# Performance work log

Measured on AMD Instinct MI355X. Metric: run time of the kernel, lower is better.

The kernel has to match this reference:

```python
import jax, jax.numpy as jnp
import numpy as np

B, N, L, H = 4, 512, 512, 8
D = 64          # d_model
TAU = 4         # conv dilation
E = 25          # conv kernel size (odd, floor(100/tau))
K = 32          # low_rank_d == top-k
L_OUT = L - TAU * (E - 1)   # 416, n_manifold_embed
EPS = 1e-6


def setup_inputs() -> dict:
    key = jax.random.key(0)
    ks = jax.random.split(key, 7)
    return {
        "x": jax.random.normal(ks[0], (B, N, L, H), jnp.float32),
        "target": jax.random.normal(ks[1], (B, N, L), jnp.float32),
        "conv_w": jax.random.normal(ks[2], (D, H, E), jnp.float32) * 0.05,  # Conv1d weight (out,in,k)
        "proj_w": jax.random.normal(ks[3], (L_OUT,), jnp.float32) * 0.05,   # Linear(L_OUT,1) weight
        "proj_b": jnp.zeros((), jnp.float32),                                # Linear bias
        "W0": jax.random.normal(ks[4], (L, K), jnp.float32) * 0.05,          # low-rank corr proj
        "U0": jax.random.normal(ks[5], (L, K), jnp.float32) * 0.05,
    }


def reference(x, target, conv_w, proj_w, proj_b, W0, U0):
    # --- dilated conv1d manifold embedding: (b n l h) -> ((b n) h l) ---
    xin = jnp.transpose(x.reshape(B * N, L, H), (0, 2, 1))  # (BN, H, L)
    conv = jax.lax.conv_general_dilated(
        xin, conv_w, window_strides=(1,), padding="VALID",
        rhs_dilation=(TAU,), dimension_numbers=("NCH", "OIH", "NCH"))  # (BN, D, L_OUT)
    # conv_out_proj: Linear(L_OUT -> 1) + GELU (exact erf, torch default)
    embed = jax.nn.gelu(conv @ proj_w + proj_b, approximate=False).reshape(B, N, D)

    # --- pearson correlation (computed under no_grad in torch) ---
    v = target - target.mean(axis=-1, keepdims=True)          # (B, N, L)
    vx = v @ W0                                               # (B, N, K)
    vh = v @ U0                                               # (B, N, K)
    num = jnp.einsum("bnk,bmk->bnm", vx, vh)                  # (B, N, N)
    nx = jnp.sqrt(jnp.sum(vx * vx, axis=-1) + EPS)            # (B, N)
    nh = jnp.sqrt(jnp.sum(vh * vh, axis=-1) + EPS)
    pearson = jax.lax.stop_gradient(num / (nx[:, :, None] * nh[:, None, :]))

    # --- top-k sparsification + scatter + softmax normalization ---
    vals, idx = jax.lax.top_k(pearson, K)                     # (B, N, K)
    bi = jnp.arange(B)[:, None, None]
    ni = jnp.arange(N)[None, :, None]
    sparse = jnp.zeros_like(pearson).at[bi, ni, idx].set(vals)  # scatter topk values
    mult = jax.nn.softmax(sparse, axis=-1)                    # F.softmax over full row (zeros included)

    # --- gated attention: sparse correlation graph mixes manifold embeddings ---
    out = jnp.einsum("bnm,bmd->bnd", mult, embed)             # (B, N, D)
    attn = pearson.mean(axis=0)                               # (N, N), returned pearson_cor
    return out, attn
```

## Files before the change

kernel.cpp:

```cpp
#include <hip/hip_runtime.h>
#include <math.h>

#define BB 4
#define NN 512
#define LL 512
#define HH 8
#define DD 64
#define EE 25
#define KK 32
#define LOUT 416
#define EPSF 1e-6f


__global__ void k_transpose_cw(const float* __restrict__ cw, float* __restrict__ Ct) {
    int i = blockIdx.x * 256 + threadIdx.x;
    if (i < DD * HH * EE) {
        int d = i / (HH * EE);
        int he = i % (HH * EE);
        Ct[he * DD + d] = cw[i];
    }
}

__global__ __launch_bounds__(256, 4) void k_fused(
    const float* __restrict__ x, const float* __restrict__ pw,
    const float* __restrict__ pb, const float* __restrict__ Ct,
    float* __restrict__ embedBuf,
    const float* __restrict__ target, const float* __restrict__ W0,
    const float* __restrict__ U0, float* __restrict__ vxn,
    float* __restrict__ vhnT) {
    __shared__ float P[608];
    __shared__ float Sred[4][200];
    __shared__ float Stot[200];
    __shared__ float opart[4][64];
    __shared__ float T[2][512];
    __shared__ float mus[2];
    __shared__ float S2[4][2][64];

    int tid = threadIdx.x;
    int w = tid >> 6, lane = tid & 63;
    int bid = blockIdx.x;
    int sel = bid % 3;

    if (sel != 2) {
        int bn = (bid / 3) * 2 + sel;
        for (int i = tid; i < 608; i += 256) {
            int t = i - 96;
            P[i] = (t >= 0 && t < LOUT) ? pw[t] : 0.f;
        }
        __syncthreads();

        const float* xp = x + (size_t)bn * (LL * HH);
        int q = lane >> 3;
        int jb = 16 * w;

        float W[25];
#pragma unroll
        for (int k = 0; k < 25; ++k) W[k] = P[q + 8 * jb + 4 * k];
        float S[25];
#pragma unroll
        for (int e = 0; e < 25; ++e) S[e] = 0.f;

#pragma unroll
        for (int jl = 0; jl < 16; ++jl) {
            int j = jb + jl;
            float v = xp[64 * j + lane];
#pragma unroll
            for (int k = 0; k < 25; ++k)
                S[24 - k] = fmaf(v, W[k], S[24 - k]);
            if (jl < 15) {
#pragma unroll
                for (int k = 0; k < 23; ++k) W[k] = W[k + 2];
                int l = q + 8 * j;
                W[23] = P[l + 100];
                W[24] = P[l + 104];
            }
        }
#pragma unroll
        for (int e = 0; e < 25; ++e) {
            S[e] += __shfl_xor(S[e], 8);
            S[e] += __shfl_xor(S[e], 16);
            S[e] += __shfl_xor(S[e], 32);
        }
        if (lane < 8) {
#pragma unroll
            for (int e = 0; e < 25; ++e) Sred[w][lane * 25 + e] = S[e];
        }
        __syncthreads();
        if (tid < 200)
            Stot[tid] = Sred[0][tid] + Sred[1][tid] + Sred[2][tid] + Sred[3][tid];
        __syncthreads();

        float acc = 0.f;
#pragma unroll 10
        for (int ii = 0; ii < 50; ++ii) {
            int i = 50 * w + ii;
            acc = fmaf(Ct[i * 64 + lane], Stot[i], acc);
        }
        opart[w][lane] = acc;
        __syncthreads();
        if (w == 0) {
            float a = opart[0][lane] + opart[1][lane] + opart[2][lane]
                    + opart[3][lane] + pb[0];
            float g = 0.5f * a * (1.f + erff(a * 0.70710678118654752f));
            embedBuf[(size_t)bn * 64 + lane] = g;
        }
    } else {
        int r0 = (bid / 3) * 2;
        const float4* tp = (const float4*)(target + (size_t)r0 * 512);
        ((float4*)&T[0][0])[tid] = tp[tid];
        __syncthreads();

        if (w < 2) {
            float s = 0.f;
#pragma unroll
            for (int c = 0; c < 8; ++c) s += T[w][lane + 64 * c];
#pragma unroll
            for (int off = 1; off < 64; off <<= 1) s += __shfl_xor(s, off);
            if (lane == 0) mus[w] = s * (1.f / 512.f);
        }
        __syncthreads();
#pragma unroll
        for (int c = 0; c < 4; ++c) {
            int i = tid + c * 256;
            T[i >> 9][i & 511] -= mus[i >> 9];
        }
        __syncthreads();

        const float* base = (lane < 32) ? W0 : U0;
        int k = lane & 31;
        float acc0 = 0.f, acc1 = 0.f;
        int l0 = w * 128;
#pragma unroll 4
        for (int li = 0; li < 128; ++li) {
            int l = l0 + li;
            float wv = base[l * 32 + k];
            acc0 = fmaf(wv, T[0][l], acc0);
            acc1 = fmaf(wv, T[1][l], acc1);
        }
        S2[w][0][lane] = acc0;
        S2[w][1][lane] = acc1;
        __syncthreads();

        if (w < 2) {
            int r = w;
            float tot = S2[0][r][lane] + S2[1][r][lane] + S2[2][r][lane]
                      + S2[3][r][lane];
            float sq = tot * tot;
#pragma unroll
            for (int off = 1; off < 32; off <<= 1) sq += __shfl_xor(sq, off);
            float o = tot / sqrtf(sq + EPSF);
            int row = r0 + r, b = row >> 9, n = row & 511;
            if (lane < 32) vxn[(size_t)row * 32 + lane] = o;
            else           vhnT[(size_t)b * (32 * 512) + (lane - 32) * 512 + n] = o;
        }
    }
}

__global__ __launch_bounds__(1024) void k_sumembed(
    const float* __restrict__ embedBuf, float* __restrict__ sumEmbed) {
    int b = blockIdx.x, tid = threadIdx.x;
    int d = tid & 63, c = tid >> 6;
    float s = 0.f;
    for (int r = c; r < 512; r += 16)
        s += embedBuf[((size_t)b * 512 + r) * 64 + d];
    __shared__ float red[16][64];
    red[c][d] = s;
    __syncthreads();
    if (c == 0) {
        float t = 0.f;
#pragma unroll
        for (int j = 0; j < 16; ++j) t += red[j][d];
        sumEmbed[b * 64 + d] = t;
    }
}

__device__ __forceinline__ unsigned long long mkkey(float v, int m) {
    unsigned u = __float_as_uint(v);
    u = (u & 0x80000000u) ? ~u : (u | 0x80000000u);
    return ((unsigned long long)u << 9) | (unsigned)(511 - m);
}

__global__ __launch_bounds__(256, 8) void k_attn(
    const float* __restrict__ vxn, const float* __restrict__ vhnT,
    const float* __restrict__ embedBuf, const float* __restrict__ sumEmbed,
    float* __restrict__ outO, float* __restrict__ pbuf) {
    __shared__ float candVal[128];
    __shared__ int   candIdx[128];
    __shared__ float sSelVal[32];
    __shared__ int   sSelIdx[32];
    __shared__ float opart[4][64];
    __shared__ float esum[4];
    __shared__ float sM[1];
    int tid = threadIdx.x, w = tid >> 6, lane = tid & 63;
    int bid = blockIdx.x;
    int b = bid >> 9, n = bid & 511;

    const float* vxp = vxn + ((size_t)(b * 512 + n)) * 32;
    float xk[32];
#pragma unroll
    for (int k = 0; k < 32; ++k)
        xk[k] = __uint_as_float(__builtin_amdgcn_readfirstlane(
                    __float_as_uint(vxp[k])));

    int m0 = w * 128 + lane;
    const float* vt = vhnT + (size_t)b * (32 * 512);
    float a0 = 0.f, a1 = 0.f;
#pragma unroll
    for (int k = 0; k < 32; ++k) {
        float v0 = vt[k * 512 + m0];
        float v1 = vt[k * 512 + m0 + 64];
        a0 = fmaf(xk[k], v0, a0);
        a1 = fmaf(xk[k], v1, a1);
    }
    float* pr = pbuf + ((size_t)(b * 512 + n)) * 512;
    pr[m0] = a0;
    pr[m0 + 64] = a1;

    unsigned long long k0 = mkkey(a0, m0), k1 = mkkey(a1, m0 + 64);
    unsigned long long prefix = 0ull;
    for (int bit = 40; bit >= 0; --bit) {
        unsigned long long cand = prefix | (1ull << bit);
        int cnt = __popcll(__ballot(k0 >= cand)) + __popcll(__ballot(k1 >= cand));
        if (cnt >= KK) prefix = cand;
    }
    bool s0 = (k0 >= prefix), s1 = (k1 >= prefix);
    unsigned long long b0 = __ballot(s0), b1 = __ballot(s1);
    unsigned long long lm = lane ? (~0ull >> (64 - lane)) : 0ull;
    int basec = w * 32;
    if (s0) { int sl = basec + __popcll(b0 & lm); candVal[sl] = a0; candIdx[sl] = m0; }
    if (s1) { int sl = basec + __popcll(b0) + __popcll(b1 & lm);
              candVal[sl] = a1; candIdx[sl] = m0 + 64; }
    __syncthreads();

    if (w == 0) {
        float v0 = candVal[lane],  v1 = candVal[64 + lane];
        int   i0 = candIdx[lane],  i1 = candIdx[64 + lane];
        unsigned long long c0 = mkkey(v0, i0), c1 = mkkey(v1, i1);
        unsigned long long pfx = 0ull;
        for (int bit = 40; bit >= 0; --bit) {
            unsigned long long cand = pfx | (1ull << bit);
            int cnt = __popcll(__ballot(c0 >= cand)) + __popcll(__ballot(c1 >= cand));
            if (cnt >= KK) pfx = cand;
        }
        bool t0 = (c0 >= pfx), t1 = (c1 >= pfx);
        unsigned long long d0 = __ballot(t0), d1 = __ballot(t1);
        if (t0) { int sl = __popcll(d0 & lm); sSelVal[sl] = v0; sSelIdx[sl] = i0; }
        if (t1) { int sl = __popcll(d0) + __popcll(d1 & lm);
                  sSelVal[sl] = v1; sSelIdx[sl] = i1; }
        float mx = fmaxf(v0, v1);
#pragma unroll
        for (int off = 1; off < 64; off <<= 1) mx = fmaxf(mx, __shfl_xor(mx, off));
        if (lane == 0) sM[0] = fmaxf(mx, 0.f);
    }
    __syncthreads();

    float M = sM[0];
    float enM = __expf(-M);
    float oacc = 0.f, es = 0.f;
    const float* eb = embedBuf + (size_t)b * 512 * 64;
#pragma unroll
    for (int i = 0; i < 8; ++i) {
        int idx = sSelIdx[w * 8 + i];
        float wv = __expf(sSelVal[w * 8 + i] - M);
        es += wv;
        oacc = fmaf(wv - enM, eb[(size_t)idx * 64 + lane], oacc);
    }
    opart[w][lane] = oacc;
    if (lane == 0) esum[w] = es;
    __syncthreads();
    if (w == 0) {
        float o = opart[0][lane] + opart[1][lane] + opart[2][lane] + opart[3][lane];
        float E = esum[0] + esum[1] + esum[2] + esum[3] + (float)(NN - KK) * enM;
        o = fmaf(enM, sumEmbed[b * 64 + lane], o);
        outO[((size_t)(b * 512 + n)) * 64 + lane] = o / E;
    }
}

__global__ __launch_bounds__(256) void k_mean(
    const float* __restrict__ pbuf, float* __restrict__ outA) {
    int i = blockIdx.x * 256 + threadIdx.x;
    float s = pbuf[i] + pbuf[262144 + i] + pbuf[524288 + i] + pbuf[786432 + i];
    outA[i] = 0.25f * s;
}

extern "C" void kernel_launch(void* const* d_in, const int* in_sizes, int n_in,
                              void* d_out, int out_size, void* d_ws, size_t ws_size,
                              hipStream_t stream) {
    const float* x      = (const float*)d_in[0];
    const float* target = (const float*)d_in[1];
    const float* cw     = (const float*)d_in[2];
    const float* pw     = (const float*)d_in[3];
    const float* pb     = (const float*)d_in[4];
    const float* W0     = (const float*)d_in[5];
    const float* U0     = (const float*)d_in[6];

    float* out  = (float*)d_out;
    float* attn = out + 4 * 512 * 64;

    float* ws       = (float*)d_ws;
    float* embedBuf = ws;
    float* sumEmbed = ws + 131072;
    float* vxn      = ws + 131328;
    float* vhnT     = ws + 196864;
    float* Ct       = ws + 262400;
    float* pbuf     = ws + 275200;

    k_transpose_cw<<<50, 256, 0, stream>>>(cw, Ct);
    k_fused<<<3072, 256, 0, stream>>>(x, pw, pb, Ct, embedBuf,
                                      target, W0, U0, vxn, vhnT);
    k_sumembed<<<4, 1024, 0, stream>>>(embedBuf, sumEmbed);
    k_attn<<<2048, 256, 0, stream>>>(vxn, vhnT, embedBuf, sumEmbed, out, pbuf);
    k_mean<<<1024, 256, 0, stream>>>(pbuf, attn);
}
```

Measured before the change: 135.4 us.

## Fold embedding column-sum into attention launch and defer background term to final kernel

Removes the standalone column-sum kernel. Four extra blocks in the attention launch now compute the per-batch embedding sums, and each row stores its enM/E coefficient. A new final kernel does the vectorized float4 pearson batch mean and adds coef*sumEmbed to the output rows. This drops one launch and the serial dependency, at the cost of an extra read-modify-write pass over the output and a small coefficient buffer.

```diff
diff --git a/kernel.cpp b/kernel.cpp
--- a/kernel.cpp
+++ b/kernel.cpp
@@ -156,24 +156,6 @@
     }
 }
 
-__global__ __launch_bounds__(1024) void k_sumembed(
-    const float* __restrict__ embedBuf, float* __restrict__ sumEmbed) {
-    int b = blockIdx.x, tid = threadIdx.x;
-    int d = tid & 63, c = tid >> 6;
-    float s = 0.f;
-    for (int r = c; r < 512; r += 16)
-        s += embedBuf[((size_t)b * 512 + r) * 64 + d];
-    __shared__ float red[16][64];
-    red[c][d] = s;
-    __syncthreads();
-    if (c == 0) {
-        float t = 0.f;
-#pragma unroll
-        for (int j = 0; j < 16; ++j) t += red[j][d];
-        sumEmbed[b * 64 + d] = t;
-    }
-}
-
 __device__ __forceinline__ unsigned long long mkkey(float v, int m) {
     unsigned u = __float_as_uint(v);
     u = (u & 0x80000000u) ? ~u : (u | 0x80000000u);
@@ -182,8 +164,9 @@
 
 __global__ __launch_bounds__(256, 8) void k_attn(
     const float* __restrict__ vxn, const float* __restrict__ vhnT,
-    const float* __restrict__ embedBuf, const float* __restrict__ sumEmbed,
-    float* __restrict__ outO, float* __restrict__ pbuf) {
+    const float* __restrict__ embedBuf, float* __restrict__ sumEmbed,
+    float* __restrict__ outO, float* __restrict__ pbuf,
+    float* __restrict__ coef) {
     __shared__ float candVal[128];
     __shared__ int   candIdx[128];
     __shared__ float sSelVal[32];
@@ -193,6 +176,21 @@
     __shared__ float sM[1];
     int tid = threadIdx.x, w = tid >> 6, lane = tid & 63;
     int bid = blockIdx.x;
+
+    if (bid >= 2048) {
+        int b = bid - 2048;
+        int d = tid & 63, c = tid >> 6;
+        float s = 0.f;
+        for (int r = c; r < 512; r += 4)
+            s += embedBuf[((size_t)b * 512 + r) * 64 + d];
+        __shared__ float red[4][64];
+        red[c][d] = s;
+        __syncthreads();
+        if (c == 0)
+            sumEmbed[b * 64 + d] = red[0][d] + red[1][d] + red[2][d] + red[3][d];
+        return;
+    }
+
     int b = bid >> 9, n = bid & 511;
 
     const float* vxp = vxn + ((size_t)(b * 512 + n)) * 32;
@@ -271,16 +269,34 @@
     if (w == 0) {
         float o = opart[0][lane] + opart[1][lane] + opart[2][lane] + opart[3][lane];
         float E = esum[0] + esum[1] + esum[2] + esum[3] + (float)(NN - KK) * enM;
-        o = fmaf(enM, sumEmbed[b * 64 + lane], o);
         outO[((size_t)(b * 512 + n)) * 64 + lane] = o / E;
-    }
-}
-
-__global__ __launch_bounds__(256) void k_mean(
-    const float* __restrict__ pbuf, float* __restrict__ outA) {
-    int i = blockIdx.x * 256 + threadIdx.x;
-    float s = pbuf[i] + pbuf[262144 + i] + pbuf[524288 + i] + pbuf[786432 + i];
-    outA[i] = 0.25f * s;
+        if (lane == 0) coef[b * 512 + n] = enM / E;
+    }
+}
+
+__global__ __launch_bounds__(256) void k_final(
+    const float* __restrict__ pbuf, float* __restrict__ outA,
+    const float* __restrict__ coef, const float* __restrict__ sumEmbed,
+    float* __restrict__ outO) {
+    int bid = blockIdx.x, tid = threadIdx.x;
+    if (bid < 256) {
+        int i = bid * 256 + tid;
+        const float4* p4 = (const float4*)pbuf;
+        float4 s0 = p4[i], s1 = p4[65536 + i], s2 = p4[131072 + i],
+               s3 = p4[196608 + i];
+        float4 r;
+        r.x = 0.25f * (s0.x + s1.x + s2.x + s3.x);
+        r.y = 0.25f * (s0.y + s1.y + s2.y + s3.y);
+        r.z = 0.25f * (s0.z + s1.z + s2.z + s3.z);
+        r.w = 0.25f * (s0.w + s1.w + s2.w + s3.w);
+        ((float4*)outA)[i] = r;
+    } else {
+        int rid = (bid - 256) * 4 + (tid >> 6);
+        int d = tid & 63;
+        int b = rid >> 9;
+        outO[(size_t)rid * 64 + d] =
+            fmaf(coef[rid], sumEmbed[b * 64 + d], outO[(size_t)rid * 64 + d]);
+    }
 }
 
 extern "C" void kernel_launch(void* const* d_in, const int* in_sizes, int n_in,
@@ -304,11 +320,11 @@
     float* vhnT     = ws + 196864;
     float* Ct       = ws + 262400;
     float* pbuf     = ws + 275200;
+    float* coef     = ws + 1323776;
 
     k_transpose_cw<<<50, 256, 0, stream>>>(cw, Ct);
     k_fused<<<3072, 256, 0, stream>>>(x, pw, pb, Ct, embedBuf,
                                       target, W0, U0, vxn, vhnT);
-    k_sumembed<<<4, 1024, 0, stream>>>(embedBuf, sumEmbed);
-    k_attn<<<2048, 256, 0, stream>>>(vxn, vhnT, embedBuf, sumEmbed, out, pbuf);
-    k_mean<<<1024, 256, 0, stream>>>(pbuf, attn);
-}
+    k_attn<<<2052, 256, 0, stream>>>(vxn, vhnT, embedBuf, sumEmbed, out, pbuf, coef);
+    k_final<<<768, 256, 0, stream>>>(pbuf, attn, coef, sumEmbed, out);
+}
```

Measured after the change: 136.7 us. No clear change (+0.9%).
